# Optimization experiments

Hardware: AMD Instinct MI355X
Metric: run time of the kernel (lower is better)

Reference implementation:

```python
import jax, jax.numpy as jnp
import numpy as np

B, N, D, H, K, NH = 4096, 2048, 1024, 4096, 5, 8
HD = D // NH  # head dim


def setup_inputs() -> dict:
    key = jax.random.key(0)
    ks = jax.random.split(key, 12)
    s_d = np.float32(1.0 / np.sqrt(D))
    s_h = np.float32(1.0 / np.sqrt(H))
    rn = lambda k, sh, s: jax.random.normal(k, sh, dtype=jnp.float32) * s
    return {
        "morph0": jax.random.normal(ks[0], (B, D), dtype=jnp.float32),
        "stored_morph0": jax.random.normal(ks[1], (N, D), dtype=jnp.float32),
        "stored_morph1": jax.random.normal(ks[2], (N, D), dtype=jnp.float32),
        "wq": rn(ks[3], (D, D), s_d), "bq": jnp.zeros((D,), jnp.float32),
        "wk": rn(ks[4], (D, D), s_d), "bk": jnp.zeros((D,), jnp.float32),
        "wv": rn(ks[5], (D, D), s_d), "bv": jnp.zeros((D,), jnp.float32),
        "wo": rn(ks[6], (D, D), s_d), "bo": jnp.zeros((D,), jnp.float32),
        "w1": rn(ks[7], (H, D), s_d), "b1": jnp.zeros((H,), jnp.float32),
        "w2": rn(ks[8], (H, H), s_h), "b2": jnp.zeros((H,), jnp.float32),
        "w3": rn(ks[9], (D, H), s_h), "b3": jnp.zeros((D,), jnp.float32),
    }


def _l2norm(x):
    # F.normalize(dim=1): x / max(||x||, eps)
    n = jnp.sqrt(jnp.sum(x * x, axis=-1, keepdims=True))
    return x / jnp.maximum(n, 1e-12)


def reference(morph0, stored_morph0, stored_morph1,
              wq, bq, wk, bk, wv, bv, wo, bo,
              w1, b1, w2, b2, w3, b3):
    # ---- retrieve similar patterns: cosine sim + topk + fused gather-subtract ----
    qn = _l2norm(morph0)                       # [B, D]
    sn = _l2norm(stored_morph0)                # [N, D]
    sim = qn @ sn.T                            # [B, N]
    _, top_idx = jax.lax.top_k(sim, K)         # [B, K]
    evo = stored_morph1 - stored_morph0        # [N, D]
    selected = jnp.take(evo, top_idx, axis=0)  # [B, K, D] evolution vectors

    # ---- torch.nn.MultiheadAttention(D, 8, batch_first=True), eval mode ----
    q = (morph0 @ wq.T + bq).reshape(B, 1, NH, HD)      # [B, 1, NH, HD]
    k = (selected @ wk.T + bk).reshape(B, K, NH, HD)    # [B, K, NH, HD]
    v = (selected @ wv.T + bv).reshape(B, K, NH, HD)
    scores = jnp.einsum('bqhd,bkhd->bhqk', q, k) / np.float32(np.sqrt(HD))  # [B, NH, 1, K]
    attn = jax.nn.softmax(scores, axis=-1)
    ctx = jnp.einsum('bhqk,bkhd->bqhd', attn, v).reshape(B, 1, D)
    context = (ctx @ wo.T + bo)[:, 0, :]                # [B, D]
    attn_weights = attn.mean(axis=1)                    # [B, 1, K] (avg over heads)

    # ---- evolution net (dropout inactive in eval) + residual ----
    x = morph0 + context
    h1 = jax.nn.relu(x @ w1.T + b1)
    h2 = jax.nn.relu(h1 @ w2.T + b2)
    predicted = morph0 + (h2 @ w3.T + b3)
    return predicted, attn_weights
```

## Files before the change

### kernel.cpp

```cpp
#include <hip/hip_runtime.h>
#include <hip/hip_bf16.h>
#include <math.h>

typedef __bf16 bf16_t;
typedef __bf16 bf16x4 __attribute__((ext_vector_type(4)));
typedef __bf16 bf16x8 __attribute__((ext_vector_type(8)));
typedef float  f32x4  __attribute__((ext_vector_type(4)));

#define BB 4096
#define NN 2048
#define DD 1024
#define HH 4096
#define KSEL 5
#define NHEAD 8

__device__ __forceinline__ unsigned short bfbits(float f) {
  return __builtin_bit_cast(unsigned short, (bf16_t)f);
}

__device__ __forceinline__ void gload_lds16(const void* g, void* l) {
  __builtin_amdgcn_global_load_lds(
      (const __attribute__((address_space(1))) void*)g,
      (__attribute__((address_space(3))) void*)l, 16, 0, 0);
}

__device__ __forceinline__ ushort4 cvt4(float4 x) {
  ushort4 o;
  o.x = bfbits(x.x); o.y = bfbits(x.y); o.z = bfbits(x.z); o.w = bfbits(x.w);
  return o;
}

#define P_M0   1048576
#define P_S0   1572864
#define P_EVO  2097152
#define P_WQ   2359296
#define P_WK   2621440
#define P_WV   2883584
#define P_WO   3145728
#define P_W1   4194304
#define P_W2   8388608
#define P_W3   9437184
__global__ void __launch_bounds__(256)
prep_k(const float4* __restrict__ m0, const float4* __restrict__ s0,
       const float4* __restrict__ s1,
       const float4* __restrict__ wq, const float4* __restrict__ wk,
       const float4* __restrict__ wv, const float4* __restrict__ wo,
       const float4* __restrict__ w1, const float4* __restrict__ w2,
       const float4* __restrict__ w3,
       ushort4* __restrict__ m0b, ushort4* __restrict__ s0b,
       ushort4* __restrict__ evo,
       ushort4* __restrict__ wqb, ushort4* __restrict__ wkb,
       ushort4* __restrict__ wvb, ushort4* __restrict__ wob,
       ushort4* __restrict__ w1b, ushort4* __restrict__ w2b,
       ushort4* __restrict__ w3b)
{
  const int stride = gridDim.x * 256;
  for (int i = blockIdx.x * 256 + threadIdx.x; i < P_W3; i += stride) {
    if (i < P_M0) {
      m0b[i] = cvt4(m0[i]);
    } else if (i < P_S0) {
      int j = i - P_M0; s0b[j] = cvt4(s0[j]);
    } else if (i < P_EVO) {
      int j = i - P_S0;
      float4 a = s0[j], b = s1[j];
      float4 d; d.x = b.x - a.x; d.y = b.y - a.y; d.z = b.z - a.z; d.w = b.w - a.w;
      evo[j] = cvt4(d);
    } else if (i < P_WQ) {
      int j = i - P_EVO; wqb[j] = cvt4(wq[j]);
    } else if (i < P_WK) {
      int j = i - P_WQ; wkb[j] = cvt4(wk[j]);
    } else if (i < P_WV) {
      int j = i - P_WK; wvb[j] = cvt4(wv[j]);
    } else if (i < P_WO) {
      int j = i - P_WV; wob[j] = cvt4(wo[j]);
    } else if (i < P_W1) {
      int j = i - P_WO; w1b[j] = cvt4(w1[j]);
    } else if (i < P_W2) {
      int j = i - P_W1; w2b[j] = cvt4(w2[j]);
    } else {
      int j = i - P_W2; w3b[j] = cvt4(w3[j]);
    }
  }
}

__global__ void rnormd_k(const float* __restrict__ s0, double* __restrict__ rnd) {
  __shared__ double red[256];
  int n = blockIdx.x, tid = threadIdx.x;
  const float4* row = (const float4*)(s0 + (size_t)n * DD);
  float4 x = row[tid];
  double ss = (double)x.x * x.x + (double)x.y * x.y + (double)x.z * x.z + (double)x.w * x.w;
  red[tid] = ss; __syncthreads();
  for (int s = 128; s > 0; s >>= 1) {
    if (tid < s) red[tid] += red[tid + s];
    __syncthreads();
  }
  if (tid == 0) rnd[n] = 1.0 / fmax(sqrt(red[0]), 1e-12);
}

template<bool RELU, bool RESID, bool OUTBF16>
__global__ void __launch_bounds__(256)
gemm_bt(const bf16_t* __restrict__ A, const bf16_t* __restrict__ Bw,
        const float* __restrict__ bias, const float* __restrict__ resid,
        float* __restrict__ outf, bf16_t* __restrict__ outb,
        int M, int Nn, int Kk)
{
  __shared__ alignas(16) bf16_t At[2][4096];
  __shared__ alignas(16) bf16_t Bt[2][4096];
  const int tid = threadIdx.x;
  const int wave = tid >> 6, lane = tid & 63;
  const int wm = wave >> 1, wn = wave & 1;
  const int bm = blockIdx.y << 7, bn = blockIdx.x << 7;

  const int srow  = (wave << 4) + (lane >> 2);
  const int scolb = (lane & 3) << 4;
  const char* pA0 = (const char*)A  + (size_t)(bm + srow) * Kk * 2 + scolb;
  const char* pA1 = (const char*)A  + (size_t)(bm + srow + 64) * Kk * 2 + scolb;
  const char* pB0 = (const char*)Bw + (size_t)(bn + srow) * Kk * 2 + scolb;
  const char* pB1 = (const char*)Bw + (size_t)(bn + srow + 64) * Kk * 2 + scolb;

  f32x4 zero = {0.f, 0.f, 0.f, 0.f};
  f32x4 acc[4][4];
  #pragma unroll
  for (int i = 0; i < 4; ++i)
    #pragma unroll
    for (int j = 0; j < 4; ++j) acc[i][j] = zero;

  const int fAoff = ((wm << 6) + (lane & 15)) * 32 + ((lane >> 4) << 3);
  const int fBoff = ((wn << 6) + (lane & 15)) * 32 + ((lane >> 4) << 3);

  const int nt = Kk >> 5;
  {
    char* lA = (char*)At[0] + (wave << 10);
    char* lB = (char*)Bt[0] + (wave << 10);
    gload_lds16(pA0, lA);
    gload_lds16(pA1, lA + 4096);
    gload_lds16(pB0, lB);
    gload_lds16(pB1, lB + 4096);
  }
  __syncthreads();

  for (int t = 0; t < nt; ++t) {
    const int cur = t & 1;
    if (t + 1 < nt) {
      size_t kb = (size_t)(t + 1) << 6;
      char* lA = (char*)At[cur ^ 1] + (wave << 10);
      char* lB = (char*)Bt[cur ^ 1] + (wave << 10);
      gload_lds16(pA0 + kb, lA);
      gload_lds16(pA1 + kb, lA + 4096);
      gload_lds16(pB0 + kb, lB);
      gload_lds16(pB1 + kb, lB + 4096);
    }
    bf16x8 av[4], bv[4];
    #pragma unroll
    for (int i = 0; i < 4; ++i) av[i] = *(const bf16x8*)(&At[cur][fAoff + i * 512]);
    #pragma unroll
    for (int j = 0; j < 4; ++j) bv[j] = *(const bf16x8*)(&Bt[cur][fBoff + j * 512]);
    #pragma unroll
    for (int i = 0; i < 4; ++i)
      #pragma unroll
      for (int j = 0; j < 4; ++j)
        acc[i][j] = __builtin_amdgcn_mfma_f32_16x16x32_bf16(av[i], bv[j], acc[i][j], 0, 0, 0);
    __syncthreads();
  }

  const int r0 = bm + (wm << 6) + ((lane >> 4) << 2);
  const int c0 = bn + (wn << 6) + (lane & 15);
  #pragma unroll
  for (int i = 0; i < 4; ++i) {
    #pragma unroll
    for (int j = 0; j < 4; ++j) {
      #pragma unroll
      for (int r = 0; r < 4; ++r) {
        int row = r0 + i * 16 + r;
        int col = c0 + j * 16;
        size_t o = (size_t)row * Nn + col;
        float v = acc[i][j][r];
        if (bias)  v += bias[col];
        if (RESID) v += resid[o];
        if (RELU)  v = fmaxf(v, 0.f);
        if (OUTBF16) outb[o] = (bf16_t)v;
        else         outf[o] = v;
      }
    }
  }
}

template<bool RELU>
__global__ void __launch_bounds__(512, 2)
gemm8p(const bf16_t* __restrict__ A, const bf16_t* __restrict__ Bw,
       const float* __restrict__ bias, bf16_t* __restrict__ outb,
       int Nn, int Kk, int nbx)
{
  __shared__ alignas(16) bf16_t As[2][16384];
  __shared__ alignas(16) bf16_t Bs[2][16384];
  const int tid  = threadIdx.x;
  const int lane = tid & 63, wv = tid >> 6;
  const int wm = wv >> 2, wn = wv & 3;
  const int ln15 = lane & 15, ln4 = lane >> 4;

  const int nwg = gridDim.x;
  const int q = nwg >> 3, r = nwg & 7;
  const int xcd = blockIdx.x & 7, loc = blockIdx.x >> 3;
  const int swz = (xcd < r ? xcd * (q + 1) : r * (q + 1) + (xcd - r) * q) + loc;
  const int bm = (swz / nbx) << 8;
  const int bn = (swz % nbx) << 8;

  const int NT = Kk >> 6;

  f32x4 acc[8][4];
  f32x4 zero = {0.f, 0.f, 0.f, 0.f};
  #pragma unroll
  for (int i = 0; i < 8; ++i)
    #pragma unroll
    for (int j = 0; j < 4; ++j) acc[i][j] = zero;

  auto stageA = [&](int MH, bf16_t* lds, int kt) {
    #pragma unroll
    for (int u = 0; u < 2; ++u) {
      int rowbase = u * 128 + MH * 64 + wv * 8;
      int row = rowbase + (lane >> 3);
      int slot = (lane & 7) ^ (row & 7);
      gload_lds16(A + (size_t)(bm + row) * Kk + kt * 64 + slot * 8,
                  (char*)lds + rowbase * 128);
    }
  };
  auto stageB = [&](int NH, bf16_t* lds, int kt) {
    #pragma unroll
    for (int u = 0; u < 2; ++u) {
      int rowbase = u * 128 + ((wv >> 2) << 6) + NH * 32 + ((wv & 3) << 3);
      int row = rowbase + (lane >> 3);
      int slot = (lane & 7) ^ (row & 7);
      gload_lds16(Bw + (size_t)(bn + row) * Kk + kt * 64 + slot * 8,
                  (char*)lds + rowbase * 128);
    }
  };

  stageA(0, As[0], 0); stageA(1, As[0], 0);
  stageB(0, Bs[0], 0); stageB(1, Bs[0], 0);
  asm volatile("s_waitcnt vmcnt(0)" ::: "memory");
  __builtin_amdgcn_s_barrier();

#define DS_A(MH)                                                                 \
    _Pragma("unroll") for (int mi = 0; mi < 4; ++mi)                             \
      _Pragma("unroll") for (int kk = 0; kk < 2; ++kk) {                         \
        const int row = wm * 128 + (MH) * 64 + mi * 16 + ln15;                   \
        const int slot = kk * 4 + ln4;                                           \
        av[mi][kk] = *(const bf16x8*)(Ab + row * 128 + ((slot ^ (row & 7)) << 4)); \
      }
#define DS_B(NH)                                                                 \
    _Pragma("unroll") for (int nj = 0; nj < 2; ++nj)                             \
      _Pragma("unroll") for (int kk = 0; kk < 2; ++kk) {                         \
        const int row = wn * 64 + (NH) * 32 + nj * 16 + ln15;                    \
        const int slot = kk * 4 + ln4;                                           \
        bv[nj][kk] = *(const bf16x8*)(Bb + row * 128 + ((slot ^ (row & 7)) << 4)); \
      }
#define MMA(MH, NH)                                                              \
    __builtin_amdgcn_s_setprio(1);                                               \
    _Pragma("unroll") for (int kk = 0; kk < 2; ++kk)                             \
      _Pragma("unroll") for (int mi = 0; mi < 4; ++mi)                           \
        _Pragma("unroll") for (int nj = 0; nj < 2; ++nj)                         \
          acc[(MH)*4+mi][(NH)*2+nj] = __builtin_amdgcn_mfma_f32_16x16x32_bf16(   \
              av[mi][kk], bv[nj][kk], acc[(MH)*4+mi][(NH)*2+nj], 0, 0, 0);       \
    __builtin_amdgcn_s_setprio(0);
#define VMW4                                                                     \
    asm volatile("s_waitcnt vmcnt(4)" ::: "memory");                             \
    __builtin_amdgcn_sched_barrier(0);

  for (int t = 0; t < NT; ++t) {
    const int cur = t & 1;
    const char* Ab = (const char*)As[cur];
    const char* Bb = (const char*)Bs[cur];
    bf16_t* nA = As[cur ^ 1];
    bf16_t* nB = Bs[cur ^ 1];
    const bool more = (t + 1 < NT);
    bf16x8 av[4][2], bv[2][2];

    DS_A(0); DS_B(0);
    if (more) stageA(0, nA, t + 1);
    __builtin_amdgcn_s_barrier();
    MMA(0, 0);
    VMW4;
    __builtin_amdgcn_s_barrier();

    DS_A(1);
    if (more) stageB(0, nB, t + 1);
    __builtin_amdgcn_s_barrier();
    MMA(1, 0);
    VMW4;
    __builtin_amdgcn_s_barrier();

    DS_A(0); DS_B(1);
    if (more) stageA(1, nA, t + 1);
    __builtin_amdgcn_s_barrier();
    MMA(0, 1);
    __builtin_amdgcn_s_barrier();

    DS_A(1);
    if (more) stageB(1, nB, t + 1);
    __builtin_amdgcn_s_barrier();
    MMA(1, 1);
    VMW4;
    __builtin_amdgcn_s_barrier();
  }
#undef DS_A
#undef DS_B
#undef MMA
#undef VMW4

  #pragma unroll
  for (int am = 0; am < 8; ++am) {
    #pragma unroll
    for (int an = 0; an < 4; ++an) {
      #pragma unroll
      for (int rr = 0; rr < 4; ++rr) {
        int row = bm + wm * 128 + am * 16 + (lane >> 4) * 4 + rr;
        int col = bn + wn * 64 + an * 16 + ln15;
        float v = acc[am][an][rr] + bias[col];
        if (RELU) v = fmaxf(v, 0.f);
        outb[(size_t)row * Nn + col] = (bf16_t)v;
      }
    }
  }
}

__global__ void __launch_bounds__(256)
topk8_k(const float* __restrict__ sim, const double* __restrict__ rnd,
        int* __restrict__ cand)
{
  __shared__ float vals[NN];
  __shared__ float rv[256];
  __shared__ int   ri[256];
  int b = blockIdx.x, tid = threadIdx.x;
  for (int t = 0; t < NN / 256; ++t) {
    int i = tid + t * 256;
    vals[i] = sim[(size_t)b * NN + i] * (float)rnd[i];
  }
  __syncthreads();
  for (int p = 0; p < 8; ++p) {
    float bvv = -INFINITY; int bi = NN;
    for (int t = 0; t < NN / 256; ++t) {
      int i = tid + t * 256;
      float v = vals[i];
      if (v > bvv) { bvv = v; bi = i; }
    }
    rv[tid] = bvv; ri[tid] = bi;
    __syncthreads();
    for (int s = 128; s > 0; s >>= 1) {
      if (tid < s) {
        float v2 = rv[tid + s]; int i2 = ri[tid + s];
        if (v2 > rv[tid] || (v2 == rv[tid] && i2 < ri[tid])) { rv[tid] = v2; ri[tid] = i2; }
      }
      __syncthreads();
    }
    if (tid == 0) {
      int wsel = ri[0];
      cand[b * 8 + p] = wsel;
      vals[wsel] = -INFINITY;
    }
    __syncthreads();
  }
}

__global__ void __launch_bounds__(256)
refine_k(const float* __restrict__ m0, const float* __restrict__ s0,
         const double* __restrict__ rnd, const int* __restrict__ cand,
         int* __restrict__ topidx)
{
  __shared__ double red[256];
  __shared__ double vals[8];
  int b = blockIdx.x, tid = threadIdx.x;
  int cs[8];
  #pragma unroll
  for (int j = 0; j < 8; ++j) cs[j] = cand[b * 8 + j];
  const float* q = m0 + (size_t)b * DD;
  double part[8];
  #pragma unroll
  for (int j = 0; j < 8; ++j) part[j] = 0.0;
  for (int d = tid; d < DD; d += 256) {
    double qd = (double)q[d];
    #pragma unroll
    for (int j = 0; j < 8; ++j)
      part[j] += qd * (double)s0[(size_t)cs[j] * DD + d];
  }
  for (int j = 0; j < 8; ++j) {
    red[tid] = part[j]; __syncthreads();
    for (int s = 128; s > 0; s >>= 1) {
      if (tid < s) red[tid] += red[tid + s];
      __syncthreads();
    }
    if (tid == 0) vals[j] = red[0] * rnd[cs[j]];
    __syncthreads();
  }
  if (tid == 0) {
    bool used[8] = {false,false,false,false,false,false,false,false};
    for (int p = 0; p < KSEL; ++p) {
      int best = -1;
      for (int j = 0; j < 8; ++j) {
        if (used[j]) continue;
        if (best < 0 || vals[j] > vals[best] ||
            (vals[j] == vals[best] && cs[j] < cs[best])) best = j;
      }
      used[best] = true;
      topidx[b * KSEL + p] = cs[best];
    }
  }
}

__global__ void __launch_bounds__(256)
attn_k(const bf16_t* __restrict__ q, const bf16_t* __restrict__ eK,
       const bf16_t* __restrict__ eV, const int* __restrict__ tidx,
       bf16_t* __restrict__ ctx, float* __restrict__ attn_out)
{
  __shared__ float aw[NHEAD][KSEL];
  const int b = blockIdx.x, t = threadIdx.x;
  const int d0 = t << 2;
  int idx[KSEL];
  #pragma unroll
  for (int j = 0; j < KSEL; ++j) idx[j] = tidx[b * KSEL + j];

  bf16x4 qv = *(const bf16x4*)(q + (size_t)b * DD + d0);
  float s[KSEL];
  #pragma unroll
  for (int j = 0; j < KSEL; ++j) {
    bf16x4 kv = *(const bf16x4*)(eK + (size_t)idx[j] * DD + d0);
    float p = (float)qv[0] * (float)kv[0] + (float)qv[1] * (float)kv[1]
            + (float)qv[2] * (float)kv[2] + (float)qv[3] * (float)kv[3];
    #pragma unroll
    for (int m = 16; m > 0; m >>= 1) p += __shfl_xor(p, m);
    s[j] = p * 0.08838834764831845f;
  }
  float mx = s[0];
  #pragma unroll
  for (int j = 1; j < KSEL; ++j) mx = fmaxf(mx, s[j]);
  float e[KSEL], sum = 0.f;
  #pragma unroll
  for (int j = 0; j < KSEL; ++j) { e[j] = expf(s[j] - mx); sum += e[j]; }
  float inv = 1.f / sum;

  float c0 = 0.f, c1 = 0.f, c2 = 0.f, c3 = 0.f;
  #pragma unroll
  for (int j = 0; j < KSEL; ++j) {
    float a = e[j] * inv;
    bf16x4 vv = *(const bf16x4*)(eV + (size_t)idx[j] * DD + d0);
    c0 += a * (float)vv[0]; c1 += a * (float)vv[1];
    c2 += a * (float)vv[2]; c3 += a * (float)vv[3];
    if ((t & 31) == 0) aw[t >> 5][j] = a;
  }
  bf16x4 co; co[0] = (bf16_t)c0; co[1] = (bf16_t)c1; co[2] = (bf16_t)c2; co[3] = (bf16_t)c3;
  *(bf16x4*)(ctx + (size_t)b * DD + d0) = co;
  __syncthreads();
  if (t < KSEL) {
    float m = 0.f;
    #pragma unroll
    for (int hh = 0; hh < NHEAD; ++hh) m += aw[hh][t];
    attn_out[(size_t)b * KSEL + t] = m * 0.125f;
  }
}

extern "C" void kernel_launch(void* const* d_in, const int* in_sizes, int n_in,
                              void* d_out, int out_size, void* d_ws, size_t ws_size,
                              hipStream_t stream) {
  (void)in_sizes; (void)n_in; (void)out_size; (void)ws_size;
  const float* morph0 = (const float*)d_in[0];
  const float* s0     = (const float*)d_in[1];
  const float* s1     = (const float*)d_in[2];
  const float* wq = (const float*)d_in[3];  const float* bq = (const float*)d_in[4];
  const float* wk = (const float*)d_in[5];  const float* bk = (const float*)d_in[6];
  const float* wv = (const float*)d_in[7];  const float* bv = (const float*)d_in[8];
  const float* wo = (const float*)d_in[9];  const float* bo = (const float*)d_in[10];
  const float* w1 = (const float*)d_in[11]; const float* b1 = (const float*)d_in[12];
  const float* w2 = (const float*)d_in[13]; const float* b2 = (const float*)d_in[14];
  const float* w3 = (const float*)d_in[15]; const float* b3 = (const float*)d_in[16];

  char* ws = (char*)d_ws;
  size_t off = 0;
  auto alloc = [&](size_t bytes) { char* p = ws + off; off += (bytes + 255) & ~(size_t)255; return p; };

  float*  sim  = (float*) alloc((size_t)BB * NN * 4);
  bf16_t* m0b  = (bf16_t*)alloc((size_t)BB * DD * 2);
  bf16_t* s0b  = (bf16_t*)alloc((size_t)NN * DD * 2);
  bf16_t* evo  = (bf16_t*)alloc((size_t)NN * DD * 2);
  double* rnd  = (double*)alloc((size_t)NN * 8);
  int*    cand = (int*)   alloc((size_t)BB * 8 * 4);
  int*    tidx = (int*)   alloc((size_t)BB * KSEL * 4);
  bf16_t* qb   = (bf16_t*)alloc((size_t)BB * DD * 2);
  bf16_t* eKb  = (bf16_t*)alloc((size_t)NN * DD * 2);
  bf16_t* eVb  = (bf16_t*)alloc((size_t)NN * DD * 2);
  bf16_t* ctxb = (bf16_t*)alloc((size_t)BB * DD * 2);
  bf16_t* xb   = (bf16_t*)alloc((size_t)BB * DD * 2);
  bf16_t* wqb  = (bf16_t*)alloc((size_t)DD * DD * 2);
  bf16_t* wkb  = (bf16_t*)alloc((size_t)DD * DD * 2);
  bf16_t* wvb  = (bf16_t*)alloc((size_t)DD * DD * 2);
  bf16_t* wob  = (bf16_t*)alloc((size_t)DD * DD * 2);
  bf16_t* w1b  = (bf16_t*)alloc((size_t)HH * DD * 2);
  bf16_t* w2b  = (bf16_t*)alloc((size_t)HH * HH * 2);
  bf16_t* w3b  = (bf16_t*)alloc((size_t)DD * HH * 2);
  bf16_t* h2b  = (bf16_t*)alloc((size_t)BB * HH * 2);
  bf16_t* h1b  = (bf16_t*)sim;
  float*  attn_out = (float*)d_out + (size_t)BB * DD;

  prep_k<<<dim3(2048), dim3(256), 0, stream>>>(
      (const float4*)morph0, (const float4*)s0, (const float4*)s1,
      (const float4*)wq, (const float4*)wk, (const float4*)wv, (const float4*)wo,
      (const float4*)w1, (const float4*)w2, (const float4*)w3,
      (ushort4*)m0b, (ushort4*)s0b, (ushort4*)evo,
      (ushort4*)wqb, (ushort4*)wkb, (ushort4*)wvb, (ushort4*)wob,
      (ushort4*)w1b, (ushort4*)w2b, (ushort4*)w3b);
  rnormd_k<<<dim3(NN), dim3(256), 0, stream>>>(s0, rnd);

  gemm_bt<false,false,false><<<dim3(NN/128, BB/128), dim3(256), 0, stream>>>(
      m0b, s0b, nullptr, nullptr, sim, nullptr, BB, NN, DD);
  topk8_k<<<dim3(BB), dim3(256), 0, stream>>>(sim, rnd, cand);
  refine_k<<<dim3(BB), dim3(256), 0, stream>>>(morph0, s0, rnd, cand, tidx);

  gemm_bt<false,false,true><<<dim3(DD/128, BB/128), dim3(256), 0, stream>>>(
      m0b, wqb, bq, nullptr, nullptr, qb, BB, DD, DD);
  gemm_bt<false,false,true><<<dim3(DD/128, NN/128), dim3(256), 0, stream>>>(
      evo, wkb, bk, nullptr, nullptr, eKb, NN, DD, DD);
  gemm_bt<false,false,true><<<dim3(DD/128, NN/128), dim3(256), 0, stream>>>(
      evo, wvb, bv, nullptr, nullptr, eVb, NN, DD, DD);

  attn_k<<<dim3(BB), dim3(256), 0, stream>>>(qb, eKb, eVb, tidx, ctxb, attn_out);

  gemm_bt<false,true,true><<<dim3(DD/128, BB/128), dim3(256), 0, stream>>>(
      ctxb, wob, bo, morph0, nullptr, xb, BB, DD, DD);

  gemm8p<true><<<dim3((BB/256)*(HH/256)), dim3(512), 0, stream>>>(
      xb, w1b, b1, h1b, HH, DD, HH/256);
  gemm8p<true><<<dim3((BB/256)*(HH/256)), dim3(512), 0, stream>>>(
      h1b, w2b, b2, h2b, HH, HH, HH/256);
  gemm_bt<false,true,false><<<dim3(DD/128, BB/128), dim3(256), 0, stream>>>(
      h2b, w3b, b3, morph0, (float*)d_out, nullptr, BB, DD, HH);
}
```

Measured before the change: 549.2 us.

## Reorder GEMM main loop to split phases by K half instead of N half

Each 64-wide K tile of the bf16 MFMA GEMM is now processed as two 32-wide K slices, with all four N fragments loaded at once rather than splitting the work by N half. This halves the A-fragment LDS reads per tile and shrinks the fragment registers each wave holds. The order of next-tile global-to-LDS staging changes to fetch B first, then A, and the vmcnt waits are retuned to match. The risk is that the new staging order and wait points expose more global-load latency or change how well MFMA overlaps with loads.

```diff
diff --git a/kernel.cpp b/kernel.cpp
--- a/kernel.cpp
+++ b/kernel.cpp
@@ -240,30 +240,27 @@
   asm volatile("s_waitcnt vmcnt(0)" ::: "memory");
   __builtin_amdgcn_s_barrier();
 
-#define DS_A(MH)                                                                 \
+#define DS_A(MH, KK)                                                             \
+    _Pragma("unroll") for (int mi = 0; mi < 4; ++mi) {                           \
+      const int row = wm * 128 + (MH) * 64 + mi * 16 + ln15;                     \
+      const int slot = (KK) * 4 + ln4;                                           \
+      av[mi] = *(const bf16x8*)(Ab + row * 128 + ((slot ^ (row & 7)) << 4));     \
+    }
+#define DS_B(KK)                                                                 \
+    _Pragma("unroll") for (int nj = 0; nj < 4; ++nj) {                           \
+      const int row = wn * 64 + nj * 16 + ln15;                                  \
+      const int slot = (KK) * 4 + ln4;                                           \
+      bv[nj] = *(const bf16x8*)(Bb + row * 128 + ((slot ^ (row & 7)) << 4));     \
+    }
+#define MMA(MH)                                                                  \
+    __builtin_amdgcn_s_setprio(1);                                               \
     _Pragma("unroll") for (int mi = 0; mi < 4; ++mi)                             \
-      _Pragma("unroll") for (int kk = 0; kk < 2; ++kk) {                         \
-        const int row = wm * 128 + (MH) * 64 + mi * 16 + ln15;                   \
-        const int slot = kk * 4 + ln4;                                           \
-        av[mi][kk] = *(const bf16x8*)(Ab + row * 128 + ((slot ^ (row & 7)) << 4)); \
-      }
-#define DS_B(NH)                                                                 \
-    _Pragma("unroll") for (int nj = 0; nj < 2; ++nj)                             \
-      _Pragma("unroll") for (int kk = 0; kk < 2; ++kk) {                         \
-        const int row = wn * 64 + (NH) * 32 + nj * 16 + ln15;                    \
-        const int slot = kk * 4 + ln4;                                           \
-        bv[nj][kk] = *(const bf16x8*)(Bb + row * 128 + ((slot ^ (row & 7)) << 4)); \
-      }
-#define MMA(MH, NH)                                                              \
-    __builtin_amdgcn_s_setprio(1);                                               \
-    _Pragma("unroll") for (int kk = 0; kk < 2; ++kk)                             \
-      _Pragma("unroll") for (int mi = 0; mi < 4; ++mi)                           \
-        _Pragma("unroll") for (int nj = 0; nj < 2; ++nj)                         \
-          acc[(MH)*4+mi][(NH)*2+nj] = __builtin_amdgcn_mfma_f32_16x16x32_bf16(   \
-              av[mi][kk], bv[nj][kk], acc[(MH)*4+mi][(NH)*2+nj], 0, 0, 0);       \
+      _Pragma("unroll") for (int nj = 0; nj < 4; ++nj)                           \
+        acc[(MH)*4+mi][nj] = __builtin_amdgcn_mfma_f32_16x16x32_bf16(            \
+            av[mi], bv[nj], acc[(MH)*4+mi][nj], 0, 0, 0);                        \
     __builtin_amdgcn_s_setprio(0);
-#define VMW4                                                                     \
-    asm volatile("s_waitcnt vmcnt(4)" ::: "memory");                             \
+#define VMW2                                                                     \
+    asm volatile("s_waitcnt vmcnt(2)" ::: "memory");                             \
     __builtin_amdgcn_sched_barrier(0);
 
   for (int t = 0; t < NT; ++t) {
@@ -273,39 +270,38 @@
     bf16_t* nA = As[cur ^ 1];
     bf16_t* nB = Bs[cur ^ 1];
     const bool more = (t + 1 < NT);
-    bf16x8 av[4][2], bv[2][2];
-
-    DS_A(0); DS_B(0);
+    bf16x8 av[4], bv[4];
+
+    DS_A(0, 0); DS_B(0);
+    if (more) stageB(0, nB, t + 1);
+    __builtin_amdgcn_s_barrier();
+    MMA(0);
+    VMW2;
+    __builtin_amdgcn_s_barrier();
+
+    DS_A(1, 0);
+    if (more) stageB(1, nB, t + 1);
+    __builtin_amdgcn_s_barrier();
+    MMA(1);
+    __builtin_amdgcn_s_barrier();
+
+    DS_A(0, 1); DS_B(1);
     if (more) stageA(0, nA, t + 1);
     __builtin_amdgcn_s_barrier();
-    MMA(0, 0);
-    VMW4;
-    __builtin_amdgcn_s_barrier();
-
-    DS_A(1);
-    if (more) stageB(0, nB, t + 1);
-    __builtin_amdgcn_s_barrier();
-    MMA(1, 0);
-    VMW4;
-    __builtin_amdgcn_s_barrier();
-
-    DS_A(0); DS_B(1);
+    MMA(0);
+    __builtin_amdgcn_s_barrier();
+
+    DS_A(1, 1);
     if (more) stageA(1, nA, t + 1);
     __builtin_amdgcn_s_barrier();
-    MMA(0, 1);
-    __builtin_amdgcn_s_barrier();
-
-    DS_A(1);
-    if (more) stageB(1, nB, t + 1);
-    __builtin_amdgcn_s_barrier();
-    MMA(1, 1);
-    VMW4;
+    MMA(1);
+    VMW2;
     __builtin_amdgcn_s_barrier();
   }
 #undef DS_A
 #undef DS_B
 #undef MMA
-#undef VMW4
+#undef VMW2
 
   #pragma unroll
   for (int am = 0; am < 8; ++am) {
```

After: 534.0 us. -2.8%, faster.
